# Kernel tuning notes

Hardware: AMD Instinct MI355X
Metric: run time of the kernel (lower is better)

The kernel has to match this reference:

```python
import jax, jax.numpy as jnp
import numpy as np
import math

D_MODEL = 96
D_INNER = 192
D_STATE = 16
DT_RANK = 6
K = 8
H = 64
W = 64
BATCH = 1


def _perms(h, w):
    L = h * w
    rows = math.ceil(L / (w + 1)); cols = w + 1
    flatT = np.arange(rows * cols).reshape(rows, cols).T.reshape(-1)
    scan_idx = flatT[flatT < L]          # zigzag (oblique) gather order
    inv_idx = np.argsort(scan_idx)       # inverse permutation for merge
    return scan_idx, inv_idx


def setup_inputs() -> dict:
    key = jax.random.key(0)
    ks = jax.random.split(key, 8)
    x = jax.random.normal(ks[0], (BATCH, D_MODEL, H, W), dtype=jnp.float32)
    W_in = jax.random.normal(ks[1], (2 * D_INNER, D_MODEL), dtype=jnp.float32) / np.sqrt(D_MODEL)
    conv_w = jax.random.normal(ks[2], (D_INNER, 1, 3, 3), dtype=jnp.float32) * 0.1
    conv_b = jnp.zeros((D_INNER,), dtype=jnp.float32)
    x_proj_weight = jax.random.normal(ks[3], (K, DT_RANK + 2 * D_STATE, D_INNER), dtype=jnp.float32) / np.sqrt(D_INNER)
    dt_std = DT_RANK ** -0.5
    dt_projs_weight = jax.random.uniform(ks[4], (K, D_INNER, DT_RANK), dtype=jnp.float32, minval=-dt_std, maxval=dt_std)
    rng = np.random.RandomState(0)
    dt = np.exp(rng.rand(K, D_INNER) * (math.log(0.1) - math.log(0.001)) + math.log(0.001)).clip(min=1e-4)
    dt_projs_bias = jnp.asarray(dt + np.log(-np.expm1(-dt)), dtype=jnp.float32)
    A_logs = jnp.log(jnp.tile(jnp.arange(1, D_STATE + 1, dtype=jnp.float32)[None, :], (K * D_INNER, 1)))
    Ds = jnp.ones((K * D_INNER,), dtype=jnp.float32)
    ln_g = jnp.ones((D_INNER,), dtype=jnp.float32)
    ln_b = jnp.zeros((D_INNER,), dtype=jnp.float32)
    W_out = jax.random.normal(ks[5], (D_MODEL, D_INNER), dtype=jnp.float32) / np.sqrt(D_INNER)
    return {"x": x, "W_in": W_in, "conv_w": conv_w, "conv_b": conv_b,
            "x_proj_weight": x_proj_weight, "dt_projs_weight": dt_projs_weight,
            "dt_projs_bias": dt_projs_bias, "A_logs": A_logs, "Ds": Ds,
            "ln_g": ln_g, "ln_b": ln_b, "W_out": W_out}


def reference(x, W_in, conv_w, conv_b, x_proj_weight, dt_projs_weight, dt_projs_bias, A_logs, Ds, ln_g, ln_b, W_out):
    Bsz, Cm, h, w = x.shape
    L = h * w
    d_inner = conv_w.shape[0]
    N = A_logs.shape[1]
    dt_rank = dt_projs_weight.shape[2]

    # in_proj (channels-last linear), split into x and gate z
    xz = jnp.einsum('bhwc,ec->bhwe', x.transpose(0, 2, 3, 1), W_in)
    xin, z = jnp.split(xz, 2, axis=-1)

    # depthwise conv + SiLU
    xc = xin.transpose(0, 3, 1, 2)
    xc = jax.lax.conv_general_dilated(xc, conv_w, (1, 1), 'SAME',
                                      feature_group_count=d_inner,
                                      dimension_numbers=('NCHW', 'OIHW', 'NCHW'))
    xc = jax.nn.silu(xc + conv_b[None, :, None, None])

    # ---- forward_core: build 8 directional sequences ----
    scan_idx, inv_idx = _perms(h, w)
    row_even = (np.arange(h) % 2 == 0)[None, None, :, None]
    col_even = (np.arange(w) % 2 == 0)[None, None, :, None]

    xr = jnp.where(row_even, xc, jnp.flip(xc, 3))               # snake row-major
    xt = jnp.swapaxes(xc, 2, 3)                                  # (B,C,W,H)
    xcol = jnp.where(col_even, xt, jnp.flip(xt, 3))              # snake col-major
    d0 = xr.reshape(Bsz, d_inner, L)
    d1 = xcol.reshape(Bsz, d_inner, L)
    d2 = xc.reshape(Bsz, d_inner, L)[..., scan_idx]              # oblique
    d3 = jnp.flip(xc, 3).reshape(Bsz, d_inner, L)[..., scan_idx] # anti-oblique
    xs = jnp.stack([d0, d1, d2, d3], axis=1)                     # (B,4,D,L)
    xs = jnp.concatenate([xs, jnp.flip(xs, -1)], axis=1)         # (B,8,D,L)

    # grouped projections
    x_dbl = jnp.einsum('bkdl,kcd->bkcl', xs, x_proj_weight)
    dts, Bm, Cmat = jnp.split(x_dbl, [dt_rank, dt_rank + N], axis=2)
    dts = jnp.einsum('bkrl,kdr->bkdl', dts, dt_projs_weight)

    # selective scan
    delta = jax.nn.softplus(dts + dt_projs_bias[None, :, :, None])
    A = -jnp.exp(A_logs).reshape(K, d_inner, N)
    dA = jnp.exp(jnp.einsum('bkdl,kdn->lbkdn', delta, A))
    dBu = jnp.einsum('bkdl,bknl,bkdl->lbkdn', delta, Bm, xs)

    def step(hst, ab):
        a, bu = ab
        hst = a * hst + bu
        return hst, hst

    h0 = jnp.zeros((Bsz, K, d_inner, N), dtype=xs.dtype)
    _, hs = jax.lax.scan(step, h0, (dA, dBu))                    # (L,B,K,D,N)
    y = jnp.einsum('lbkdn,bknl->bkdl', hs, Cmat)
    out_y = y + xs * Ds.reshape(K, d_inner)[None, :, :, None]    # (B,8,D,L)

    def row_unflip(v):
        return jnp.where(row_even, v, jnp.flip(v, 3)).reshape(Bsz, d_inner, L)

    def col_unflip(v):
        return jnp.swapaxes(jnp.where(col_even, v, jnp.flip(v, 3)), 2, 3).reshape(Bsz, d_inner, L)

    y1 = row_unflip(out_y[:, 0].reshape(Bsz, d_inner, h, w))
    y2 = col_unflip(out_y[:, 1].reshape(Bsz, d_inner, w, h))
    y1i = row_unflip(jnp.flip(out_y[:, 4], -1).reshape(Bsz, d_inner, h, w))
    y2i = col_unflip(jnp.flip(out_y[:, 5], -1).reshape(Bsz, d_inner, w, h))
    y3 = out_y[:, 2][..., inv_idx]
    y3i = jnp.flip(out_y[:, 6], -1)[..., inv_idx]
    y4 = jnp.flip(out_y[:, 3][..., inv_idx].reshape(Bsz, d_inner, h, w), -1).reshape(Bsz, d_inner, L)
    y4i = jnp.flip(jnp.flip(out_y[:, 7], -1)[..., inv_idx].reshape(Bsz, d_inner, h, w), -1).reshape(Bsz, d_inner, L)

    ysum = y1 + y2 + y3 + y4 + y1i + y2i + y3i + y4i             # (B,D,L)
    yh = jnp.swapaxes(ysum, 1, 2).reshape(Bsz, h, w, d_inner)

    # LayerNorm(d_inner)
    mu = yh.mean(-1, keepdims=True)
    var = ((yh - mu) ** 2).mean(-1, keepdims=True)
    yn = (yh - mu) * jax.lax.rsqrt(var + 1e-5) * ln_g + ln_b

    yo = yn * jax.nn.silu(z)
    out = jnp.einsum('bhwd,md->bhwm', yo, W_out).transpose(0, 3, 1, 2)
    return out
```

## Files before the change

kernel.cpp:

```cpp
#include <hip/hip_runtime.h>
#include <math.h>

constexpr int NL   = 4096;
constexpr int ND   = 192;
constexpr int NDM  = 96;
constexpr int NST  = 16;
constexpr int NK   = 8;
constexpr int NDT  = 6;
constexpr int NC   = 128;
constexpr int CL   = 32;

__device__ __forceinline__ int perm_p(int k, int l) {
    int l2 = (k >= 4) ? (NL - 1 - l) : l;
    int kk = k & 3;
    if (kk == 0) {
        int r = l2 >> 6, j = l2 & 63;
        return (r << 6) | ((r & 1) ? (63 - j) : j);
    } else if (kk == 1) {
        int i = l2 >> 6, j = l2 & 63;
        int jp = (i & 1) ? (63 - j) : j;
        return (jp << 6) | i;
    } else {
        int v;
        if (l2 < 64) v = l2 * 65;
        else { int q = (l2 - 64) / 63; int r = (l2 - 64) - q * 63; v = r * 65 + q + 1; }
        return (kk == 3) ? (v ^ 63) : v;
    }
}

__device__ __forceinline__ float2 pk_mul(float2 a, float2 b) {
    float2 r; r.x = a.x * b.x; r.y = a.y * b.y; return r;
}
__device__ __forceinline__ float2 pk_fma(float2 a, float2 b, float2 c) {
    float2 r; r.x = fmaf(a.x, b.x, c.x); r.y = fmaf(a.y, b.y, c.y); return r;
}
__device__ __forceinline__ float2 f2s(float s) { float2 r; r.x = s; r.y = s; return r; }

__device__ __forceinline__ void pow_tree2(float e1, float2* a2) {
    float e2 = e1 * e1, e4 = e2 * e2, e8 = e4 * e4;
    float2 a0; a0.x = e1; a0.y = e2;
    float2 e2v = f2s(e2), e4v = f2s(e4), e8v = f2s(e8);
    a2[0] = a0;
    a2[1] = pk_mul(a0, e2v);
    a2[2] = pk_mul(a0, e4v);
    a2[3] = pk_mul(a2[1], e4v);
    a2[4] = pk_mul(a0, e8v);
    a2[5] = pk_mul(a2[1], e8v);
    a2[6] = pk_mul(a2[2], e8v);
    a2[7] = pk_mul(a2[3], e8v);
}

#if defined(__HIP_DEVICE_COMPILE__)
__device__ __forceinline__ void atomic_add_f32(float* p, float v) {
    unsafeAtomicAdd(p, v);
}
#else
__device__ __forceinline__ void atomic_add_f32(float* p, float v) { atomicAdd(p, v); }
#endif

__global__ __launch_bounds__(256) void k_zero(float* __restrict__ ysum) {
    int i = blockIdx.x * 256 + threadIdx.x;
    float4 z4; z4.x = z4.y = z4.z = z4.w = 0.f;
    *(float4*)(ysum + i * 4) = z4;
}

__global__ __launch_bounds__(256) void k_inproj(const float* __restrict__ x,
                                                const float* __restrict__ Win,
                                                float* __restrict__ xin,
                                                float* __restrict__ z) {
    __shared__ float xt[96 * 64];
    int t  = threadIdx.x;
    int p0 = blockIdx.x * 64;
    int eb = blockIdx.y * 64;
    for (int idx = t; idx < 96 * 16; idx += 256) {
        int c = idx >> 4, pq = idx & 15;
        *(float4*)(xt + c * 64 + pq * 4) = *(const float4*)(x + c * NL + p0 + pq * 4);
    }
    __syncthreads();
    int pl = t & 63;
    int g  = __builtin_amdgcn_readfirstlane(t >> 6);
    int e0 = eb + g * 16;
    float acc[16];
#pragma unroll
    for (int i = 0; i < 16; ++i) acc[i] = 0.f;
#pragma unroll 4
    for (int c = 0; c < 96; ++c) {
        float xv = xt[c * 64 + pl];
#pragma unroll
        for (int i = 0; i < 16; ++i)
            acc[i] = fmaf(xv, Win[(e0 + i) * 96 + c], acc[i]);
    }
    int p = p0 + pl;
#pragma unroll
    for (int i = 0; i < 16; ++i) {
        int e = e0 + i;
        if (e < ND) xin[e * NL + p] = acc[i];
        else        z[p * ND + (e - ND)] = acc[i];
    }
}

__global__ __launch_bounds__(256) void k_conv(const float* __restrict__ xin,
                                              const float* __restrict__ cw,
                                              const float* __restrict__ cb,
                                              float* __restrict__ xc) {
    int d = blockIdx.y;
    int p = blockIdx.x * 256 + threadIdx.x;
    int r = p >> 6, c = p & 63;
    float acc = cb[d];
    const float* w  = cw + d * 9;
    const float* xi = xin + d * NL;
#pragma unroll
    for (int dr = 0; dr < 3; ++dr) {
        int rr = r + dr - 1;
        if (rr < 0 || rr >= 64) continue;
        const float* row = xi + rr * 64;
        float m0 = (c > 0)  ? row[c - 1] : 0.f;
        float m1 = row[c];
        float m2 = (c < 63) ? row[c + 1] : 0.f;
        acc = fmaf(m0, w[dr * 3 + 0],
              fmaf(m1, w[dr * 3 + 1],
              fmaf(m2, w[dr * 3 + 2], acc)));
    }
    xc[d * NL + p] = acc / (1.f + __expf(-acc));
}

__global__ __launch_bounds__(256) void k_proj(const float* __restrict__ xc,
                                              const float* __restrict__ xpw,
                                              const float* __restrict__ dtw,
                                              const float* __restrict__ dtb,
                                              float* __restrict__ delta,
                                              float* __restrict__ Bm,
                                              float* __restrict__ Cm,
                                              float* __restrict__ xct) {
    __shared__ float xt[ND * 64];
    __shared__ float dtr_s[64 * 6];
    int t  = threadIdx.x;
    int p0 = blockIdx.x * 64;
    int k  = blockIdx.y;
    for (int idx = t; idx < ND * 16; idx += 256) {
        int d = idx >> 4, pq = idx & 15;
        *(float4*)(xt + d * 64 + pq * 4) = *(const float4*)(xc + d * NL + p0 + pq * 4);
    }
    __syncthreads();
    int pl = t & 63;
    int g  = __builtin_amdgcn_readfirstlane(t >> 6);
    const float* Wk = xpw + k * 38 * ND;
    int ci[10];
#pragma unroll
    for (int i = 0; i < 10; ++i) {
        int cc = g + 4 * i;
        ci[i] = (cc > 37) ? 37 : cc;
    }
    float acc[10];
#pragma unroll
    for (int i = 0; i < 10; ++i) acc[i] = 0.f;
#pragma unroll 2
    for (int d = 0; d < ND; d += 4) {
        float x0 = xt[(d + 0) * 64 + pl];
        float x1 = xt[(d + 1) * 64 + pl];
        float x2 = xt[(d + 2) * 64 + pl];
        float x3 = xt[(d + 3) * 64 + pl];
#pragma unroll
        for (int i = 0; i < 10; ++i) {
            float4 w4 = *(const float4*)(Wk + ci[i] * ND + d);
            acc[i] = fmaf(x0, w4.x, fmaf(x1, w4.y,
                     fmaf(x2, w4.z, fmaf(x3, w4.w, acc[i]))));
        }
    }
    int p = p0 + pl;
#pragma unroll
    for (int i = 0; i < 10; ++i) {
        int cc = g + 4 * i;
        if (cc >= 38) break;
        float v = acc[i];
        if (cc < 6)       dtr_s[pl * 6 + cc] = v;
        else if (cc < 22) Bm[(k * NL + p) * 16 + (cc - 6)]  = v;
        else              Cm[(k * NL + p) * 16 + (cc - 22)] = v;
    }
    if (k == 0) {
        int g2 = t >> 6;
#pragma unroll
        for (int i = 0; i < 12; ++i) {
            int d4 = g2 * 12 + i;
            float4 v;
            v.x = xt[(d4 * 4 + 0) * 64 + pl];
            v.y = xt[(d4 * 4 + 1) * 64 + pl];
            v.z = xt[(d4 * 4 + 2) * 64 + pl];
            v.w = xt[(d4 * 4 + 3) * 64 + pl];
            *(float4*)(xct + (p0 + pl) * ND + d4 * 4) = v;
        }
    }
    __syncthreads();
    if (t < ND) {
        int d = t;
        const float* w = dtw + (k * ND + d) * 6;
        float w0 = w[0], w1 = w[1], w2 = w[2], w3 = w[3], w4 = w[4], w5 = w[5];
        float bias = dtb[k * ND + d];
        float* dout = delta + (k * NL + p0) * ND + d;
#pragma unroll 4
        for (int pp = 0; pp < 64; ++pp) {
            const float* r6 = dtr_s + pp * 6;
            float xv = bias;
            xv = fmaf(w0, r6[0], xv); xv = fmaf(w1, r6[1], xv);
            xv = fmaf(w2, r6[2], xv); xv = fmaf(w3, r6[3], xv);
            xv = fmaf(w4, r6[4], xv); xv = fmaf(w5, r6[5], xv);
            float sp = fmaxf(xv, 0.f) + __logf(1.f + __expf(-fabsf(xv)));
            dout[pp * ND] = sp;
        }
    }
}

__global__ __launch_bounds__(192) void k_scan1(const float* __restrict__ delta,
                                               const float* __restrict__ xct,
                                               const float* __restrict__ Bm,
                                               float* __restrict__ hend,
                                               float* __restrict__ sumd) {
    int d  = threadIdx.x;
    int ch = blockIdx.x;
    int k  = blockIdx.y;
    float2 h2[8];
#pragma unroll
    for (int j = 0; j < 8; ++j) h2[j] = f2s(0.f);
    float sd = 0.f;
#pragma unroll 4
    for (int i = 0; i < CL; ++i) {
        int l = ch * CL + i;
        int p = perm_p(k, l);
        float dl = delta[(k * NL + p) * ND + d];
        float u  = xct[p * ND + d];
        float2 du2 = f2s(dl * u);
        float2 a2[8];
        pow_tree2(__expf(-dl), a2);
        const float4* Bp = (const float4*)(Bm + ((k * NL + p) << 4));
        float4 B0 = Bp[0], B1 = Bp[1], B2 = Bp[2], B3 = Bp[3];
        float2 b2[8];
        b2[0].x = B0.x; b2[0].y = B0.y; b2[1].x = B0.z; b2[1].y = B0.w;
        b2[2].x = B1.x; b2[2].y = B1.y; b2[3].x = B1.z; b2[3].y = B1.w;
        b2[4].x = B2.x; b2[4].y = B2.y; b2[5].x = B2.z; b2[5].y = B2.w;
        b2[6].x = B3.x; b2[6].y = B3.y; b2[7].x = B3.z; b2[7].y = B3.w;
#pragma unroll
        for (int j = 0; j < 8; ++j)
            h2[j] = pk_fma(a2[j], h2[j], pk_mul(du2, b2[j]));
        sd += dl;
    }
    sumd[(k * NC + ch) * ND + d] = sd;
    float* ho = hend + (k * NC + ch) * 16 * ND + d;
#pragma unroll
    for (int j = 0; j < 8; ++j) {
        ho[(2 * j) * ND]     = h2[j].x;
        ho[(2 * j + 1) * ND] = h2[j].y;
    }
}

__global__ __launch_bounds__(192) void k_scan2(const float* __restrict__ hend,
                                               const float* __restrict__ sumd,
                                               const float* __restrict__ Alogs,
                                               float* __restrict__ hinit) {
    int d = threadIdx.x;
    int n = blockIdx.x;
    int k = blockIdx.y;
    float A = -__expf(Alogs[(k * ND + d) * 16 + n]);
    float H = 0.f;
    for (int c = 0; c < NC; ++c) {
        hinit[((k * NC + c) * 16 + n) * ND + d] = H;
        float sd = sumd[(k * NC + c) * ND + d];
        float he = hend[((k * NC + c) * 16 + n) * ND + d];
        H = fmaf(__expf(A * sd), H, he);
    }
}

__global__ __launch_bounds__(192) void k_scan3(const float* __restrict__ delta,
                                               const float* __restrict__ xct,
                                               const float* __restrict__ Bm,
                                               const float* __restrict__ Cm,
                                               const float* __restrict__ hinit,
                                               float* __restrict__ ysum) {
    int d  = threadIdx.x;
    int ch = blockIdx.x;
    int k  = blockIdx.y;
    const float* hp = hinit + (k * NC + ch) * 16 * ND + d;
    float2 h2[8];
#pragma unroll
    for (int j = 0; j < 8; ++j) {
        h2[j].x = hp[(2 * j) * ND];
        h2[j].y = hp[(2 * j + 1) * ND];
    }
#pragma unroll 4
    for (int i = 0; i < CL; ++i) {
        int l = ch * CL + i;
        int p = perm_p(k, l);
        float dl = delta[(k * NL + p) * ND + d];
        float u  = xct[p * ND + d];
        float2 du2 = f2s(dl * u);
        float2 a2[8];
        pow_tree2(__expf(-dl), a2);
        const float4* Bp = (const float4*)(Bm + ((k * NL + p) << 4));
        const float4* Cp = (const float4*)(Cm + ((k * NL + p) << 4));
        float4 B0 = Bp[0], B1 = Bp[1], B2 = Bp[2], B3 = Bp[3];
        float4 C0 = Cp[0], C1 = Cp[1], C2 = Cp[2], C3 = Cp[3];
        float2 b2[8], c2[8];
        b2[0].x = B0.x; b2[0].y = B0.y; b2[1].x = B0.z; b2[1].y = B0.w;
        b2[2].x = B1.x; b2[2].y = B1.y; b2[3].x = B1.z; b2[3].y = B1.w;
        b2[4].x = B2.x; b2[4].y = B2.y; b2[5].x = B2.z; b2[5].y = B2.w;
        b2[6].x = B3.x; b2[6].y = B3.y; b2[7].x = B3.z; b2[7].y = B3.w;
        c2[0].x = C0.x; c2[0].y = C0.y; c2[1].x = C0.z; c2[1].y = C0.w;
        c2[2].x = C1.x; c2[2].y = C1.y; c2[3].x = C1.z; c2[3].y = C1.w;
        c2[4].x = C2.x; c2[4].y = C2.y; c2[5].x = C2.z; c2[5].y = C2.w;
        c2[6].x = C3.x; c2[6].y = C3.y; c2[7].x = C3.z; c2[7].y = C3.w;
        float2 y2 = f2s(0.f);
#pragma unroll
        for (int j = 0; j < 8; ++j) {
            h2[j] = pk_fma(a2[j], h2[j], pk_mul(du2, b2[j]));
            y2 = pk_fma(h2[j], c2[j], y2);
        }
        atomic_add_f32(ysum + p * ND + d, y2.x + y2.y);
    }
}

__global__ __launch_bounds__(192) void k_merge(const float* __restrict__ ysum,
                                               const float* __restrict__ xct,
                                               const float* __restrict__ z,
                                               const float* __restrict__ Ds,
                                               const float* __restrict__ lng,
                                               const float* __restrict__ lnb,
                                               float* __restrict__ yo) {
    __shared__ float red1[4], red2[4];
    int d  = threadIdx.x;
    int p0 = blockIdx.x * 8;
    float dsum = 0.f;
#pragma unroll
    for (int k = 0; k < 8; ++k) dsum += Ds[k * ND + d];
    float lg = lng[d], lb = lnb[d];
    float v[8], zv[8];
#pragma unroll
    for (int pp = 0; pp < 8; ++pp) {
        int off = (p0 + pp) * ND + d;
        v[pp]  = fmaf(xct[off], dsum, ysum[off]);
        zv[pp] = z[off];
    }
    int wid = d >> 6;
#pragma unroll
    for (int pp = 0; pp < 8; ++pp) {
        float s = v[pp], s2 = v[pp] * v[pp];
#pragma unroll
        for (int o = 32; o > 0; o >>= 1) {
            s  += __shfl_down(s, o);
            s2 += __shfl_down(s2, o);
        }
        if ((d & 63) == 0) { red1[wid] = s; red2[wid] = s2; }
        __syncthreads();
        float ts  = red1[0] + red1[1] + red1[2];
        float ts2 = red2[0] + red2[1] + red2[2];
        __syncthreads();
        float mu  = ts * (1.f / 192.f);
        float var = ts2 * (1.f / 192.f) - mu * mu;
        float rs  = rsqrtf(var + 1e-5f);
        float yn  = (v[pp] - mu) * rs * lg + lb;
        float zz  = zv[pp];
        yo[(p0 + pp) * ND + d] = yn * (zz / (1.f + __expf(-zz)));
    }
}

__global__ __launch_bounds__(256) void k_outproj(const float* __restrict__ yo,
                                                 const float* __restrict__ Wout,
                                                 float* __restrict__ out) {
    __shared__ float xt[64 * 193];
    int t  = threadIdx.x;
    int p0 = blockIdx.x * 64;
    int mq = blockIdx.y;
#pragma unroll
    for (int it = 0; it < 12; ++it) {
        int idx = it * 256 + t;
        float4 v = *(const float4*)(yo + p0 * ND + idx * 4);
        int pl = idx / 48, dq = idx - pl * 48;
        float* dst = xt + pl * 193 + dq * 4;
        dst[0] = v.x; dst[1] = v.y; dst[2] = v.z; dst[3] = v.w;
    }
    __syncthreads();
    int pl = t & 63;
    int g  = __builtin_amdgcn_readfirstlane(t >> 6);
    int m0 = mq * 24 + g * 6;
    float acc[6];
#pragma unroll
    for (int i = 0; i < 6; ++i) acc[i] = 0.f;
    const float* xr = xt + pl * 193;
#pragma unroll 2
    for (int d = 0; d < ND; d += 4) {
        float x0 = xr[d + 0];
        float x1 = xr[d + 1];
        float x2 = xr[d + 2];
        float x3 = xr[d + 3];
#pragma unroll
        for (int i = 0; i < 6; ++i) {
            float4 w4 = *(const float4*)(Wout + (m0 + i) * ND + d);
            acc[i] = fmaf(x0, w4.x, fmaf(x1, w4.y,
                     fmaf(x2, w4.z, fmaf(x3, w4.w, acc[i]))));
        }
    }
#pragma unroll
    for (int i = 0; i < 6; ++i)
        out[(m0 + i) * NL + p0 + pl] = acc[i];
}

extern "C" void kernel_launch(void* const* d_in, const int* in_sizes, int n_in,
                              void* d_out, int out_size, void* d_ws, size_t ws_size,
                              hipStream_t stream) {
    const float* x    = (const float*)d_in[0];
    const float* Win  = (const float*)d_in[1];
    const float* cw   = (const float*)d_in[2];
    const float* cb   = (const float*)d_in[3];
    const float* xpw  = (const float*)d_in[4];
    const float* dtw  = (const float*)d_in[5];
    const float* dtb  = (const float*)d_in[6];
    const float* Al   = (const float*)d_in[7];
    const float* Ds   = (const float*)d_in[8];
    const float* lng  = (const float*)d_in[9];
    const float* lnb  = (const float*)d_in[10];
    const float* Wout = (const float*)d_in[11];
    float* out = (float*)d_out;

    float* fw = (float*)d_ws;
    float* xin   = fw; fw += ND * NL;
    float* xc    = fw; fw += ND * NL;
    float* xct   = fw; fw += ND * NL;
    float* zg    = fw; fw += ND * NL;
    float* Bm    = fw; fw += NK * NL * NST;
    float* Cm    = fw; fw += NK * NL * NST;
    float* delta = fw; fw += NK * NL * ND;
    float* sumd  = fw; fw += NK * NC * ND;
    float* hend  = fw; fw += NK * NC * NST * ND;
    float* hinit = fw; fw += NK * NC * NST * ND;
    float* ysum  = fw; fw += NL * ND;
    float* yo    = xin;

    size_t needed = (size_t)(fw - (float*)d_ws) * sizeof(float);
    if (ws_size < needed) return;

    k_zero<<<NL * ND / 1024, 256, 0, stream>>>(ysum);
    k_inproj<<<dim3(64, 6), 256, 0, stream>>>(x, Win, xin, zg);
    k_conv<<<dim3(16, ND), 256, 0, stream>>>(xin, cw, cb, xc);
    k_proj<<<dim3(64, NK), 256, 0, stream>>>(xc, xpw, dtw, dtb, delta, Bm, Cm, xct);
    k_scan1<<<dim3(NC, NK), 192, 0, stream>>>(delta, xct, Bm, hend, sumd);
    k_scan2<<<dim3(NST, NK), 192, 0, stream>>>(hend, sumd, Al, hinit);
    k_scan3<<<dim3(NC, NK), 192, 0, stream>>>(delta, xct, Bm, Cm, hinit, ysum);
    k_merge<<<NL / 8, 192, 0, stream>>>(ysum, xct, zg, Ds, lng, lnb, yo);
    k_outproj<<<dim3(64, 4), 256, 0, stream>>>(yo, Wout, out);
}
```

Before: 217.6 us.

## Recompute delta inside scan kernels instead of materializing it; prefetch loads; halve chunk length

Stops k_proj from writing the full (K, L, D) softplus delta tensor. It stores only the 6-wide dt-rank projections, and each scan kernel recomputes delta per element from those values plus per-thread dt weights and bias. This removes a large global write in k_proj and two large reads in the scan passes, in exchange for recomputing the softplus twice. The scan loops are also fully unrolled with software prefetch of the next step's u, B, C and dtr, and the chunk count doubles from 128 to 256 (length 32 to 16). That gives more parallel blocks but more chunk-carry state for scan2 to process.

Result: slower. 269.6 us (+23.9%).

```diff
diff --git a/kernel.cpp b/kernel.cpp
--- a/kernel.cpp
+++ b/kernel.cpp
@@ -7,8 +7,8 @@
 constexpr int NST  = 16;
 constexpr int NK   = 8;
 constexpr int NDT  = 6;
-constexpr int NC   = 128;
-constexpr int CL   = 32;
+constexpr int NC   = 256;
+constexpr int CL   = 16;
 
 __device__ __forceinline__ int perm_p(int k, int l) {
     int l2 = (k >= 4) ? (NL - 1 - l) : l;
@@ -50,6 +50,10 @@
     a2[7] = pk_mul(a2[3], e8v);
 }
 
+__device__ __forceinline__ float softplus_f(float xv) {
+    return fmaxf(xv, 0.f) + __logf(1.f + __expf(-fabsf(xv)));
+}
+
 #if defined(__HIP_DEVICE_COMPILE__)
 __device__ __forceinline__ void atomic_add_f32(float* p, float v) {
     unsafeAtomicAdd(p, v);
@@ -126,14 +130,11 @@
 
 __global__ __launch_bounds__(256) void k_proj(const float* __restrict__ xc,
                                               const float* __restrict__ xpw,
-                                              const float* __restrict__ dtw,
-                                              const float* __restrict__ dtb,
-                                              float* __restrict__ delta,
+                                              float* __restrict__ dtr,
                                               float* __restrict__ Bm,
                                               float* __restrict__ Cm,
                                               float* __restrict__ xct) {
     __shared__ float xt[ND * 64];
-    __shared__ float dtr_s[64 * 6];
     int t  = threadIdx.x;
     int p0 = blockIdx.x * 64;
     int k  = blockIdx.y;
@@ -173,7 +174,7 @@
         int cc = g + 4 * i;
         if (cc >= 38) break;
         float v = acc[i];
-        if (cc < 6)       dtr_s[pl * 6 + cc] = v;
+        if (cc < 6)       dtr[(k * NL + p) * 6 + cc]        = v;
         else if (cc < 22) Bm[(k * NL + p) * 16 + (cc - 6)]  = v;
         else              Cm[(k * NL + p) * 16 + (cc - 22)] = v;
     }
@@ -190,49 +191,51 @@
             *(float4*)(xct + (p0 + pl) * ND + d4 * 4) = v;
         }
     }
-    __syncthreads();
-    if (t < ND) {
-        int d = t;
-        const float* w = dtw + (k * ND + d) * 6;
-        float w0 = w[0], w1 = w[1], w2 = w[2], w3 = w[3], w4 = w[4], w5 = w[5];
-        float bias = dtb[k * ND + d];
-        float* dout = delta + (k * NL + p0) * ND + d;
-#pragma unroll 4
-        for (int pp = 0; pp < 64; ++pp) {
-            const float* r6 = dtr_s + pp * 6;
-            float xv = bias;
-            xv = fmaf(w0, r6[0], xv); xv = fmaf(w1, r6[1], xv);
-            xv = fmaf(w2, r6[2], xv); xv = fmaf(w3, r6[3], xv);
-            xv = fmaf(w4, r6[4], xv); xv = fmaf(w5, r6[5], xv);
-            float sp = fmaxf(xv, 0.f) + __logf(1.f + __expf(-fabsf(xv)));
-            dout[pp * ND] = sp;
-        }
-    }
-}
-
-__global__ __launch_bounds__(192) void k_scan1(const float* __restrict__ delta,
-                                               const float* __restrict__ xct,
+}
+
+__global__ __launch_bounds__(192) void k_scan1(const float* __restrict__ xct,
                                                const float* __restrict__ Bm,
+                                               const float* __restrict__ dtr,
+                                               const float* __restrict__ dtw,
+                                               const float* __restrict__ dtb,
                                                float* __restrict__ hend,
                                                float* __restrict__ sumd) {
     int d  = threadIdx.x;
     int ch = blockIdx.x;
     int k  = blockIdx.y;
+    const float* wp = dtw + (k * ND + d) * 6;
+    float w0 = wp[0], w1 = wp[1], w2 = wp[2], w3 = wp[3], w4 = wp[4], w5 = wp[5];
+    float bias = dtb[k * ND + d];
     float2 h2[8];
 #pragma unroll
     for (int j = 0; j < 8; ++j) h2[j] = f2s(0.f);
     float sd = 0.f;
-#pragma unroll 4
+    int l0 = ch * CL;
+    int p = perm_p(k, l0);
+    float u = xct[p * ND + d];
+    const float4* Bp = (const float4*)(Bm + ((k * NL + p) << 4));
+    float4 B0 = Bp[0], B1 = Bp[1], B2 = Bp[2], B3 = Bp[3];
+    const float* rp = dtr + (k * NL + p) * 6;
+    float r0 = rp[0], r1 = rp[1], r2 = rp[2], r3 = rp[3], r4 = rp[4], r5 = rp[5];
+#pragma unroll
     for (int i = 0; i < CL; ++i) {
-        int l = ch * CL + i;
-        int p = perm_p(k, l);
-        float dl = delta[(k * NL + p) * ND + d];
-        float u  = xct[p * ND + d];
+        float un = u; float4 N0 = B0, N1 = B1, N2 = B2, N3 = B3;
+        float s0 = r0, s1 = r1, s2 = r2, s3 = r3, s4 = r4, s5 = r5;
+        if (i + 1 < CL) {
+            int pn = perm_p(k, l0 + i + 1);
+            un = xct[pn * ND + d];
+            const float4* Bn = (const float4*)(Bm + ((k * NL + pn) << 4));
+            N0 = Bn[0]; N1 = Bn[1]; N2 = Bn[2]; N3 = Bn[3];
+            const float* rn = dtr + (k * NL + pn) * 6;
+            s0 = rn[0]; s1 = rn[1]; s2 = rn[2]; s3 = rn[3]; s4 = rn[4]; s5 = rn[5];
+        }
+        float xv = bias;
+        xv = fmaf(w0, r0, xv); xv = fmaf(w1, r1, xv); xv = fmaf(w2, r2, xv);
+        xv = fmaf(w3, r3, xv); xv = fmaf(w4, r4, xv); xv = fmaf(w5, r5, xv);
+        float dl = softplus_f(xv);
         float2 du2 = f2s(dl * u);
         float2 a2[8];
         pow_tree2(__expf(-dl), a2);
-        const float4* Bp = (const float4*)(Bm + ((k * NL + p) << 4));
-        float4 B0 = Bp[0], B1 = Bp[1], B2 = Bp[2], B3 = Bp[3];
         float2 b2[8];
         b2[0].x = B0.x; b2[0].y = B0.y; b2[1].x = B0.z; b2[1].y = B0.w;
         b2[2].x = B1.x; b2[2].y = B1.y; b2[3].x = B1.z; b2[3].y = B1.w;
@@ -242,6 +245,8 @@
         for (int j = 0; j < 8; ++j)
             h2[j] = pk_fma(a2[j], h2[j], pk_mul(du2, b2[j]));
         sd += dl;
+        u = un; B0 = N0; B1 = N1; B2 = N2; B3 = N3;
+        r0 = s0; r1 = s1; r2 = s2; r3 = s3; r4 = s4; r5 = s5;
     }
     sumd[(k * NC + ch) * ND + d] = sd;
     float* ho = hend + (k * NC + ch) * 16 * ND + d;
@@ -269,15 +274,20 @@
     }
 }
 
-__global__ __launch_bounds__(192) void k_scan3(const float* __restrict__ delta,
-                                               const float* __restrict__ xct,
+__global__ __launch_bounds__(192) void k_scan3(const float* __restrict__ xct,
                                                const float* __restrict__ Bm,
                                                const float* __restrict__ Cm,
+                                               const float* __restrict__ dtr,
+                                               const float* __restrict__ dtw,
+                                               const float* __restrict__ dtb,
                                                const float* __restrict__ hinit,
                                                float* __restrict__ ysum) {
     int d  = threadIdx.x;
     int ch = blockIdx.x;
     int k  = blockIdx.y;
+    const float* wp = dtw + (k * ND + d) * 6;
+    float w0 = wp[0], w1 = wp[1], w2 = wp[2], w3 = wp[3], w4 = wp[4], w5 = wp[5];
+    float bias = dtb[k * ND + d];
     const float* hp = hinit + (k * NC + ch) * 16 * ND + d;
     float2 h2[8];
 #pragma unroll
@@ -285,19 +295,39 @@
         h2[j].x = hp[(2 * j) * ND];
         h2[j].y = hp[(2 * j + 1) * ND];
     }
-#pragma unroll 4
+    int l0 = ch * CL;
+    int p = perm_p(k, l0);
+    float u = xct[p * ND + d];
+    const float4* Bp = (const float4*)(Bm + ((k * NL + p) << 4));
+    float4 B0 = Bp[0], B1 = Bp[1], B2 = Bp[2], B3 = Bp[3];
+    const float4* Cp = (const float4*)(Cm + ((k * NL + p) << 4));
+    float4 C0 = Cp[0], C1 = Cp[1], C2 = Cp[2], C3 = Cp[3];
+    const float* rp = dtr + (k * NL + p) * 6;
+    float r0 = rp[0], r1 = rp[1], r2 = rp[2], r3 = rp[3], r4 = rp[4], r5 = rp[5];
+#pragma unroll
     for (int i = 0; i < CL; ++i) {
-        int l = ch * CL + i;
-        int p = perm_p(k, l);
-        float dl = delta[(k * NL + p) * ND + d];
-        float u  = xct[p * ND + d];
+        int pc = p;
+        float un = u; float4 N0 = B0, N1 = B1, N2 = B2, N3 = B3;
+        float4 M0 = C0, M1 = C1, M2 = C2, M3 = C3;
+        float s0 = r0, s1 = r1, s2 = r2, s3 = r3, s4 = r4, s5 = r5;
+        if (i + 1 < CL) {
+            int pn = perm_p(k, l0 + i + 1);
+            p = pn;
+            un = xct[pn * ND + d];
+            const float4* Bn = (const float4*)(Bm + ((k * NL + pn) << 4));
+            N0 = Bn[0]; N1 = Bn[1]; N2 = Bn[2]; N3 = Bn[3];
+            const float4* Cn = (const float4*)(Cm + ((k * NL + pn) << 4));
+            M0 = Cn[0]; M1 = Cn[1]; M2 = Cn[2]; M3 = Cn[3];
+            const float* rn = dtr + (k * NL + pn) * 6;
+            s0 = rn[0]; s1 = rn[1]; s2 = rn[2]; s3 = rn[3]; s4 = rn[4]; s5 = rn[5];
+        }
+        float xv = bias;
+        xv = fmaf(w0, r0, xv); xv = fmaf(w1, r1, xv); xv = fmaf(w2, r2, xv);
+        xv = fmaf(w3, r3, xv); xv = fmaf(w4, r4, xv); xv = fmaf(w5, r5, xv);
+        float dl = softplus_f(xv);
         float2 du2 = f2s(dl * u);
         float2 a2[8];
         pow_tree2(__expf(-dl), a2);
-        const float4* Bp = (const float4*)(Bm + ((k * NL + p) << 4));
-        const float4* Cp = (const float4*)(Cm + ((k * NL + p) << 4));
-        float4 B0 = Bp[0], B1 = Bp[1], B2 = Bp[2], B3 = Bp[3];
-        float4 C0 = Cp[0], C1 = Cp[1], C2 = Cp[2], C3 = Cp[3];
         float2 b2[8], c2[8];
         b2[0].x = B0.x; b2[0].y = B0.y; b2[1].x = B0.z; b2[1].y = B0.w;
         b2[2].x = B1.x; b2[2].y = B1.y; b2[3].x = B1.z; b2[3].y = B1.w;
@@ -313,7 +343,10 @@
             h2[j] = pk_fma(a2[j], h2[j], pk_mul(du2, b2[j]));
             y2 = pk_fma(h2[j], c2[j], y2);
         }
-        atomic_add_f32(ysum + p * ND + d, y2.x + y2.y);
+        atomic_add_f32(ysum + pc * ND + d, y2.x + y2.y);
+        u = un; B0 = N0; B1 = N1; B2 = N2; B3 = N3;
+        C0 = M0; C1 = M1; C2 = M2; C3 = M3;
+        r0 = s0; r1 = s1; r2 = s2; r3 = s3; r4 = s4; r5 = s5;
     }
 }
 
@@ -426,7 +459,7 @@
     float* zg    = fw; fw += ND * NL;
     float* Bm    = fw; fw += NK * NL * NST;
     float* Cm    = fw; fw += NK * NL * NST;
-    float* delta = fw; fw += NK * NL * ND;
+    float* dtr   = fw; fw += NK * NL * NDT;
     float* sumd  = fw; fw += NK * NC * ND;
     float* hend  = fw; fw += NK * NC * NST * ND;
     float* hinit = fw; fw += NK * NC * NST * ND;
@@ -439,10 +472,10 @@
     k_zero<<<NL * ND / 1024, 256, 0, stream>>>(ysum);
     k_inproj<<<dim3(64, 6), 256, 0, stream>>>(x, Win, xin, zg);
     k_conv<<<dim3(16, ND), 256, 0, stream>>>(xin, cw, cb, xc);
-    k_proj<<<dim3(64, NK), 256, 0, stream>>>(xc, xpw, dtw, dtb, delta, Bm, Cm, xct);
-    k_scan1<<<dim3(NC, NK), 192, 0, stream>>>(delta, xct, Bm, hend, sumd);
+    k_proj<<<dim3(64, NK), 256, 0, stream>>>(xc, xpw, dtr, Bm, Cm, xct);
+    k_scan1<<<dim3(NC, NK), 192, 0, stream>>>(xct, Bm, dtr, dtw, dtb, hend, sumd);
     k_scan2<<<dim3(NST, NK), 192, 0, stream>>>(hend, sumd, Al, hinit);
-    k_scan3<<<dim3(NC, NK), 192, 0, stream>>>(delta, xct, Bm, Cm, hinit, ysum);
+    k_scan3<<<dim3(NC, NK), 192, 0, stream>>>(xct, Bm, Cm, dtr, dtw, dtb, hinit, ysum);
     k_merge<<<NL / 8, 192, 0, stream>>>(ysum, xct, zg, Ds, lng, lnb, yo);
     k_outproj<<<dim3(64, 4), 256, 0, stream>>>(yo, Wout, out);
 }
```
